# Performance work log

Hardware: AMD Instinct MI355X
Metric: run time of the kernel (lower is better)

## Reference

```python
import jax, jax.numpy as jnp
import numpy as np

N_NODES = 100000
N_EDGES = 1600000
DIM = 128
N_BUNDLES = 8
BUNDLE_DIM = 4
HIDDEN = 256
TIME = 2


def setup_inputs() -> dict:
    key = jax.random.key(0)
    ks = jax.random.split(key, 8)
    x = jax.random.normal(ks[0], (N_NODES, DIM), dtype=jnp.float32)
    node_rep = jax.random.normal(ks[1], (N_NODES, N_BUNDLES, BUNDLE_DIM, BUNDLE_DIM), dtype=jnp.float32)
    # edge list; ensure every node has out-degree >= 1 so degree norm is finite
    src_extra = jax.random.randint(ks[2], (N_EDGES - N_NODES,), 0, N_NODES)
    src = jnp.concatenate([jnp.arange(N_NODES), src_extra]).astype(jnp.int64)
    dst = jax.random.randint(ks[3], (N_EDGES,), 0, N_NODES).astype(jnp.int64)
    w1 = jax.random.normal(ks[4], (HIDDEN, DIM), dtype=jnp.float32) * (1.0 / np.sqrt(DIM))
    b1 = jnp.zeros((HIDDEN,), dtype=jnp.float32)
    w2 = jax.random.normal(ks[5], (DIM, HIDDEN), dtype=jnp.float32) * (1.0 / np.sqrt(HIDDEN))
    b2 = jnp.zeros((DIM,), dtype=jnp.float32)
    return {"x": x, "node_rep": node_rep, "src": src, "dst": dst,
            "w1": w1, "b1": b1, "w2": w2, "b2": b2}


def reference(x, node_rep, src, dst, w1, b1, w2, b2):
    n = x.shape[0]
    # out-degrees (number of edges with node as source)
    deg = jax.ops.segment_sum(jnp.ones_like(src, dtype=x.dtype), src, num_segments=n)
    # u_mul_v: per-edge product of src and dst degrees -> symmetric norm coefs
    norm_coefs = jax.lax.rsqrt(deg[src] * deg[dst])  # [E]
    # per-bundle rotation: einsum('abcd,abde->abce', node_rep, vf)
    vf = x.reshape(n, N_BUNDLES, BUNDLE_DIM, -1)
    vf = jnp.einsum('nbcd,nbde->nbce', node_rep, vf)
    h = vf.reshape(n, DIM)
    # u_mul_e_sum repeated `time` times: out[dst] += h[src] * coef
    for _ in range(TIME):
        h = jax.ops.segment_sum(h[src] * norm_coefs[:, None], dst, num_segments=n)
    # inverse rotation with transposed node_rep
    vf = h.reshape(n, N_BUNDLES, BUNDLE_DIM, -1)
    vf = jnp.einsum('nbdc,nbde->nbce', node_rep, vf)
    h = vf.reshape(n, DIM)
    # feed-forward (dropout=0, exact GELU as in torch nn.GELU default)
    h = jax.nn.gelu(h @ w1.T + b1, approximate=False)
    return h @ w2.T + b2
```

## Files before the change

### kernel.cpp

```cpp
#include <hip/hip_runtime.h>
#include <hip/hip_bf16.h>
#include <math.h>

#define DIM 128
#define HID 256

typedef short s8x __attribute__((ext_vector_type(8)));
typedef float f4x __attribute__((ext_vector_type(4)));

__device__ __forceinline__ unsigned short f2bf(float f) {
    unsigned int u = __float_as_uint(f);
    u += 0x7FFF + ((u >> 16) & 1);
    return (unsigned short)(u >> 16);
}
__device__ __forceinline__ float bf2f(unsigned short b) {
    return __uint_as_float(((unsigned int)b) << 16);
}
__device__ __forceinline__ float bflo(unsigned int p) {
    return __uint_as_float(p << 16);
}
__device__ __forceinline__ float bfhi(unsigned int p) {
    return __uint_as_float(p & 0xffff0000u);
}


__global__ __launch_bounds__(256) void hist_kernel(
        const int* __restrict__ src, const int* __restrict__ dst,
        int* __restrict__ TD, int* __restrict__ TS, int nE, int nbuck, int chunk,
        int NBE) {
    __shared__ int hd[1024], hs[1024];
    const int tid = threadIdx.x, blk = blockIdx.x;
    for (int b = tid; b < nbuck; b += 256) { hd[b] = 0; hs[b] = 0; }
    __syncthreads();
    int beg = blk * chunk, end = min(beg + chunk, nE);
    for (int i = beg + tid; i < end; i += 256) {
        atomicAdd(&hd[dst[i] >> 7], 1);
        atomicAdd(&hs[src[i] >> 7], 1);
    }
    __syncthreads();
    for (int b = tid; b < nbuck; b += 256) {
        TD[b * NBE + blk] = hd[b];
        TS[b * NBE + blk] = hs[b];
    }
}

__global__ void scan_blocks(const int* in, int* out, int* bsums, int n) {
    __shared__ int part[256];
    const int tid = threadIdx.x;
    const int base = blockIdx.x * 1024 + tid * 4;
    int v[4];
    int sum = 0;
#pragma unroll
    for (int k = 0; k < 4; ++k) {
        v[k] = (base + k < n) ? in[base + k] : 0;
        sum += v[k];
    }
    part[tid] = sum;
    __syncthreads();
    for (int off = 1; off < 256; off <<= 1) {
        int t = (tid >= off) ? part[tid - off] : 0;
        __syncthreads();
        part[tid] += t;
        __syncthreads();
    }
    int excl = part[tid] - sum;
    if (tid == 255) bsums[blockIdx.x] = part[255];
#pragma unroll
    for (int k = 0; k < 4; ++k) {
        if (base + k < n) out[base + k] = excl;
        excl += v[k];
    }
}

__global__ void scan_sums(int* bsums, int nb) {
    __shared__ int part[256];
    const int tid = threadIdx.x;
    const int base = tid * 8;
    int v[8];
    int sum = 0;
#pragma unroll
    for (int k = 0; k < 8; ++k) {
        v[k] = (base + k < nb) ? bsums[base + k] : 0;
        sum += v[k];
    }
    part[tid] = sum;
    __syncthreads();
    for (int off = 1; off < 256; off <<= 1) {
        int t = (tid >= off) ? part[tid - off] : 0;
        __syncthreads();
        part[tid] += t;
        __syncthreads();
    }
    int excl = part[tid] - sum;
#pragma unroll
    for (int k = 0; k < 8; ++k) {
        if (base + k < nb) bsums[base + k] = excl;
        excl += v[k];
    }
}

__global__ void scan_add(int* T, const int* __restrict__ bsums, int n2, int half, int E) {
    int i = blockIdx.x * blockDim.x + threadIdx.x;
    if (i < n2) {
        int v = T[i] + bsums[i >> 10];
        T[i] = (i >= half) ? v - E : v;
    }
}

__global__ __launch_bounds__(256) void scatter_edges(
        const int* __restrict__ src, const int* __restrict__ dst,
        const int* __restrict__ TD, const int* __restrict__ TS,
        unsigned int* __restrict__ pairs, unsigned char* __restrict__ sbyte,
        int nE, int nbuck, int chunk, int NBE) {
    __shared__ int cd[1024], cs[1024];
    const int tid = threadIdx.x, blk = blockIdx.x;
    for (int b = tid; b < nbuck; b += 256) {
        cd[b] = TD[b * NBE + blk];
        cs[b] = TS[b * NBE + blk];
    }
    __syncthreads();
    int beg = blk * chunk, end = min(beg + chunk, nE);
    for (int i = beg + tid; i < end; i += 256) {
        int s = src[i], d = dst[i];
        int pd = atomicAdd(&cd[d >> 7], 1);
        pairs[pd] = ((unsigned)s << 7) | (unsigned)(d & 127);
        int ps = atomicAdd(&cs[s >> 7], 1);
        sbyte[ps] = (unsigned char)(s & 127);
    }
}

__global__ __launch_bounds__(256) void finalize_src(
        const unsigned char* __restrict__ sbyte, const int* __restrict__ TS,
        float* __restrict__ rdeg, int nE, int nbuck, int nN, int NBE) {
    __shared__ int hist[128];
    const int tid = threadIdx.x, b = blockIdx.x;
    if (tid < 128) hist[tid] = 0;
    __syncthreads();
    int beg = TS[b * NBE];
    int end = (b + 1 < nbuck) ? TS[(b + 1) * NBE] : nE;
    for (int i = beg + tid; i < end; i += 256)
        atomicAdd(&hist[sbyte[i]], 1);
    __syncthreads();
    if (tid < 128) {
        int idx = (b << 7) + tid;
        if (idx < nN) rdeg[idx] = rsqrtf((float)hist[tid]);
    }
}

template<bool PACK>
__global__ __launch_bounds__(256) void finalize_dst(
        const unsigned int* __restrict__ pairs, const int* __restrict__ TD,
        const float* __restrict__ rdeg,
        int* __restrict__ rowstart, uint2* __restrict__ ecsr,
        int* __restrict__ esrcA, int nE, int nbuck, int nN, int NBE) {
    __shared__ int hist[128], sbuf[128], cur[128];
    const int tid = threadIdx.x, b = blockIdx.x;
    int beg = TD[b * NBE];
    int end = (b + 1 < nbuck) ? TD[(b + 1) * NBE] : nE;
    if (tid < 128) hist[tid] = 0;
    __syncthreads();
    for (int i = beg + tid; i < end; i += 256)
        atomicAdd(&hist[(int)(pairs[i] & 127u)], 1);
    __syncthreads();
    int v = (tid < 128) ? hist[tid] : 0;
    if (tid < 128) sbuf[tid] = v;
    __syncthreads();
    for (int off = 1; off < 128; off <<= 1) {
        int t = (tid < 128 && tid >= off) ? sbuf[tid - off] : 0;
        __syncthreads();
        if (tid < 128) sbuf[tid] += t;
        __syncthreads();
    }
    if (tid < 128) {
        int excl = sbuf[tid] - v;
        cur[tid] = excl;
        int idx = (b << 7) + tid;
        if (idx <= nN) rowstart[idx] = beg + excl;
    }
    __syncthreads();
    for (int i = beg + tid; i < end; i += 256) {
        unsigned int p = pairs[i];
        int l = (int)(p & 127u);
        int s = (int)(p >> 7);
        int pos = atomicAdd(&cur[l], 1);
        if (PACK) {
            float coef = rdeg[s] * rdeg[(b << 7) + l];
            ecsr[beg + pos] = make_uint2((unsigned)s, __float_as_uint(coef));
        } else {
            esrcA[beg + pos] = s;
        }
    }
}

__global__ void rot_cvt_kernel(const float* __restrict__ x, const float* __restrict__ R,
                               unsigned short* __restrict__ h0,
                               const float* __restrict__ w1, const float* __restrict__ w2,
                               unsigned short* __restrict__ w1b, unsigned short* __restrict__ w2b,
                               int n, int nbRot) {
    if ((int)blockIdx.x >= nbRot) {
        int t = (blockIdx.x - nbRot) * 256 + threadIdx.x;
        for (int i = t; i < 32768; i += 4096) {
            w1b[i] = f2bf(w1[i]);
            w2b[i] = f2bf(w2[i]);
        }
        return;
    }
    int u = blockIdx.x * blockDim.x + threadIdx.x;
    if (u >= n * 8) return;
    int nd = u >> 3, b = u & 7;
    const float* xp = &x[(size_t)nd * DIM + b * 16];
    const float* Rp = &R[(size_t)nd * DIM + b * 16];
    float xv[16], rv[16];
#pragma unroll
    for (int d = 0; d < 4; ++d) {
        *(float4*)&xv[d * 4] = *(const float4*)&xp[d * 4];
        *(float4*)&rv[d * 4] = *(const float4*)&Rp[d * 4];
    }
    unsigned short ob[16];
#pragma unroll
    for (int c = 0; c < 4; ++c)
#pragma unroll
        for (int e = 0; e < 4; ++e) {
            float acc = 0.f;
#pragma unroll
            for (int d = 0; d < 4; ++d) acc += rv[c * 4 + d] * xv[d * 4 + e];
            ob[c * 4 + e] = f2bf(acc);
        }
    unsigned short* op = &h0[(size_t)nd * DIM + b * 16];
    *(s8x*)&op[0] = *(s8x*)&ob[0];
    *(s8x*)&op[8] = *(s8x*)&ob[8];
}

template<bool PACK>
__global__ __launch_bounds__(256) void gather_kernel(
        const unsigned short* __restrict__ hsrc,
        const uint2* __restrict__ ecsr, const int* __restrict__ esrcA,
        const float* __restrict__ rdeg, const int* __restrict__ rowstart,
        unsigned short* __restrict__ hdst, int n) {
    const int node = blockIdx.x * 16 + (threadIdx.x >> 4);
    const int lane = threadIdx.x & 15;
    if (node >= n) return;
    const int beg = rowstart[node];
    const int end = rowstart[node + 1];
    float rd = 0.f;
    if (!PACK) rd = rdeg[node];
    float a0 = 0.f, a1 = 0.f, a2 = 0.f, a3 = 0.f;
    float a4 = 0.f, a5 = 0.f, a6 = 0.f, a7 = 0.f;
    int i = beg;
    for (; i + 4 <= end; i += 4) {
        int s0, s1, s2, s3;
        float c0, c1, c2, c3;
        if (PACK) {
            uint2 e0 = ecsr[i], e1 = ecsr[i + 1], e2 = ecsr[i + 2], e3 = ecsr[i + 3];
            s0 = (int)e0.x; c0 = __uint_as_float(e0.y);
            s1 = (int)e1.x; c1 = __uint_as_float(e1.y);
            s2 = (int)e2.x; c2 = __uint_as_float(e2.y);
            s3 = (int)e3.x; c3 = __uint_as_float(e3.y);
        } else {
            s0 = esrcA[i]; s1 = esrcA[i + 1]; s2 = esrcA[i + 2]; s3 = esrcA[i + 3];
            c0 = rdeg[s0] * rd; c1 = rdeg[s1] * rd;
            c2 = rdeg[s2] * rd; c3 = rdeg[s3] * rd;
        }
        uint4 p0 = *(const uint4*)&hsrc[(size_t)s0 * DIM + lane * 8];
        uint4 p1 = *(const uint4*)&hsrc[(size_t)s1 * DIM + lane * 8];
        uint4 p2 = *(const uint4*)&hsrc[(size_t)s2 * DIM + lane * 8];
        uint4 p3 = *(const uint4*)&hsrc[(size_t)s3 * DIM + lane * 8];
        a0 += bflo(p0.x) * c0 + bflo(p1.x) * c1 + bflo(p2.x) * c2 + bflo(p3.x) * c3;
        a1 += bfhi(p0.x) * c0 + bfhi(p1.x) * c1 + bfhi(p2.x) * c2 + bfhi(p3.x) * c3;
        a2 += bflo(p0.y) * c0 + bflo(p1.y) * c1 + bflo(p2.y) * c2 + bflo(p3.y) * c3;
        a3 += bfhi(p0.y) * c0 + bfhi(p1.y) * c1 + bfhi(p2.y) * c2 + bfhi(p3.y) * c3;
        a4 += bflo(p0.z) * c0 + bflo(p1.z) * c1 + bflo(p2.z) * c2 + bflo(p3.z) * c3;
        a5 += bfhi(p0.z) * c0 + bfhi(p1.z) * c1 + bfhi(p2.z) * c2 + bfhi(p3.z) * c3;
        a6 += bflo(p0.w) * c0 + bflo(p1.w) * c1 + bflo(p2.w) * c2 + bflo(p3.w) * c3;
        a7 += bfhi(p0.w) * c0 + bfhi(p1.w) * c1 + bfhi(p2.w) * c2 + bfhi(p3.w) * c3;
    }
    for (; i < end; ++i) {
        int s0;
        float c0;
        if (PACK) {
            uint2 e0 = ecsr[i];
            s0 = (int)e0.x; c0 = __uint_as_float(e0.y);
        } else {
            s0 = esrcA[i];
            c0 = rdeg[s0] * rd;
        }
        uint4 p0 = *(const uint4*)&hsrc[(size_t)s0 * DIM + lane * 8];
        a0 += bflo(p0.x) * c0;
        a1 += bfhi(p0.x) * c0;
        a2 += bflo(p0.y) * c0;
        a3 += bfhi(p0.y) * c0;
        a4 += bflo(p0.z) * c0;
        a5 += bfhi(p0.z) * c0;
        a6 += bflo(p0.w) * c0;
        a7 += bfhi(p0.w) * c0;
    }
    uint4 o;
    o.x = (unsigned)f2bf(a0) | ((unsigned)f2bf(a1) << 16);
    o.y = (unsigned)f2bf(a2) | ((unsigned)f2bf(a3) << 16);
    o.z = (unsigned)f2bf(a4) | ((unsigned)f2bf(a5) << 16);
    o.w = (unsigned)f2bf(a6) | ((unsigned)f2bf(a7) << 16);
    *(uint4*)&hdst[(size_t)node * DIM + lane * 8] = o;
}

#define ABST 136
#define HBST 264
__global__ __launch_bounds__(256, 6) void ffn_kernel(
        const unsigned short* __restrict__ h,
        const float* __restrict__ R,
        const unsigned short* __restrict__ w1b,
        const float* __restrict__ b1,
        const unsigned short* __restrict__ w2b,
        const float* __restrict__ b2,
        float* __restrict__ out, int n) {
    __shared__ unsigned short smem[32 * HBST];
    unsigned short* abuf = smem;
    unsigned short* hbuf = smem;
    const int tid  = threadIdx.x;
    const int node0 = blockIdx.x * 32;
    const int wave = tid >> 6;
    const int lane = tid & 63;
    const int lr = lane & 15;
    const int lq = lane >> 4;

    {
        int nd = tid >> 3, b = tid & 7;
        int gn = node0 + nd;
        float hv[16], rv[16];
        if (gn < n) {
            const unsigned short* hp = &h[(size_t)gn * DIM + b * 16];
            const float* Rp = &R[(size_t)gn * DIM + b * 16];
            unsigned short hraw[16];
            *(s8x*)&hraw[0] = *(const s8x*)&hp[0];
            *(s8x*)&hraw[8] = *(const s8x*)&hp[8];
#pragma unroll
            for (int d = 0; d < 16; ++d) hv[d] = bf2f(hraw[d]);
#pragma unroll
            for (int d = 0; d < 4; ++d)
                *(float4*)&rv[d * 4] = *(const float4*)&Rp[d * 4];
        } else {
#pragma unroll
            for (int d = 0; d < 16; ++d) { hv[d] = 0.f; rv[d] = 0.f; }
        }
#pragma unroll
        for (int c = 0; c < 4; ++c) {
            unsigned short gb[4];
#pragma unroll
            for (int e = 0; e < 4; ++e) {
                float acc = 0.f;
#pragma unroll
                for (int d = 0; d < 4; ++d) acc += rv[d * 4 + c] * hv[d * 4 + e];
                gb[e] = f2bf(acc);
            }
            *(ushort4*)&abuf[nd * ABST + b * 16 + c * 4] =
                make_ushort4(gb[0], gb[1], gb[2], gb[3]);
        }
    }
    __syncthreads();

    f4x acc1[2][4];
#pragma unroll
    for (int mt = 0; mt < 2; ++mt)
#pragma unroll
        for (int nt = 0; nt < 4; ++nt) acc1[mt][nt] = (f4x){0.f, 0.f, 0.f, 0.f};

    const int nw = wave * 64;
    for (int ks = 0; ks < 4; ++ks) {
        const int k0 = ks * 32 + lq * 8;
        s8x af[2], bfv[4];
#pragma unroll
        for (int mt = 0; mt < 2; ++mt)
            af[mt] = *(const s8x*)&abuf[(mt * 16 + lr) * ABST + k0];
#pragma unroll
        for (int nt = 0; nt < 4; ++nt)
            bfv[nt] = *(const s8x*)&w1b[(size_t)(nw + nt * 16 + lr) * 128 + k0];
#pragma unroll
        for (int mt = 0; mt < 2; ++mt)
#pragma unroll
            for (int nt = 0; nt < 4; ++nt)
                acc1[mt][nt] = __builtin_amdgcn_mfma_f32_16x16x32_bf16(
                    af[mt], bfv[nt], acc1[mt][nt], 0, 0, 0);
    }
    __syncthreads();

#pragma unroll
    for (int nt = 0; nt < 4; ++nt) {
        int nn = nw + nt * 16 + lr;
        float bias = b1[nn];
#pragma unroll
        for (int mt = 0; mt < 2; ++mt) {
#pragma unroll
            for (int r = 0; r < 4; ++r) {
                float v = acc1[mt][nt][r] + bias;
                v = 0.5f * v * (1.f + erff(v * 0.70710678118654752f));
                hbuf[(mt * 16 + lq * 4 + r) * HBST + nn] = f2bf(v);
            }
        }
    }
    __syncthreads();

    f4x acc2[2][2];
#pragma unroll
    for (int mt = 0; mt < 2; ++mt)
#pragma unroll
        for (int nt = 0; nt < 2; ++nt) acc2[mt][nt] = (f4x){0.f, 0.f, 0.f, 0.f};

    const int nw2 = wave * 32;
    for (int ks = 0; ks < 8; ++ks) {
        const int k0 = ks * 32 + lq * 8;
        s8x af[2], bf2v[2];
#pragma unroll
        for (int mt = 0; mt < 2; ++mt)
            af[mt] = *(const s8x*)&hbuf[(mt * 16 + lr) * HBST + k0];
#pragma unroll
        for (int nt = 0; nt < 2; ++nt)
            bf2v[nt] = *(const s8x*)&w2b[(size_t)(nw2 + nt * 16 + lr) * 256 + k0];
#pragma unroll
        for (int mt = 0; mt < 2; ++mt)
#pragma unroll
            for (int nt = 0; nt < 2; ++nt)
                acc2[mt][nt] = __builtin_amdgcn_mfma_f32_16x16x32_bf16(
                    af[mt], bf2v[nt], acc2[mt][nt], 0, 0, 0);
    }
#pragma unroll
    for (int nt = 0; nt < 2; ++nt) {
        int n2 = nw2 + nt * 16 + lr;
        float bias = b2[n2];
#pragma unroll
        for (int mt = 0; mt < 2; ++mt) {
#pragma unroll
            for (int r = 0; r < 4; ++r) {
                int gn = node0 + mt * 16 + lq * 4 + r;
                if (gn < n) out[(size_t)gn * DIM + n2] = acc2[mt][nt][r] + bias;
            }
        }
    }
}

extern "C" void kernel_launch(void* const* d_in, const int* in_sizes, int n_in,
                              void* d_out, int out_size, void* d_ws, size_t ws_size,
                              hipStream_t stream) {
    const float* x   = (const float*)d_in[0];
    const float* R   = (const float*)d_in[1];
    const int*   src = (const int*)d_in[2];
    const int*   dst = (const int*)d_in[3];
    const float* w1  = (const float*)d_in[4];
    const float* b1  = (const float*)d_in[5];
    const float* w2  = (const float*)d_in[6];
    const float* b2  = (const float*)d_in[7];
    float* out = (float*)d_out;

    const int N = in_sizes[0] / DIM;
    const int E = in_sizes[2];

    const int nbuck = (N + 127) >> 7;

    const size_t fixed_bytes = (size_t)N * DIM * 4;
    auto tail_bytes = [&](int nbe) {
        return (size_t)N * 4 + (size_t)(N + 1) * 4 +
               (size_t)nbuck * nbe * 8 + 2048 * 4 + (size_t)2 * 32768 * 2;
    };
    int NBE = 1024;
    bool use_pack = true;
    if (fixed_bytes + (size_t)E * 8 + tail_bytes(1024) > ws_size) {
        if (fixed_bytes + (size_t)E * 8 + tail_bytes(256) <= ws_size) {
            NBE = 256;
        } else {
            NBE = 256;
            use_pack = false;
        }
    }
    const int chunk = (E + NBE - 1) / NBE;
    const int nScan = nbuck * NBE;
    const int nScan2 = 2 * nScan;
    const int nbScan2 = (nScan2 + 1023) / 1024;

    unsigned short* hA = (unsigned short*)d_ws;
    unsigned short* hM = hA + (size_t)N * DIM;
    unsigned int*  pairs = (unsigned int*)hM;
    unsigned char* sbyte = (unsigned char*)(pairs + E);
    char* edge_base = (char*)(hM + (size_t)N * DIM);
    const size_t edge_bytes = use_pack ? (size_t)E * 8 : (size_t)E * 4;

    uint2* ecsr  = (uint2*)edge_base;
    int*   esrcA = (int*)edge_base;
    char* q = edge_base + edge_bytes;
    float* rdeg     = (float*)q;
    int*   rowstart = (int*)(rdeg + N);
    int*   TD       = rowstart + (N + 1);
    int*   TS       = TD + nScan;
    int*   bsums    = TS + nScan;
    unsigned short* w1b = (unsigned short*)(bsums + 2048);
    unsigned short* w2b = w1b + 32768;

    const int BLK = 256;

    hist_kernel<<<NBE, BLK, 0, stream>>>(src, dst, TD, TS, E, nbuck, chunk, NBE);
    scan_blocks<<<nbScan2, BLK, 0, stream>>>(TD, TD, bsums, nScan2);
    scan_sums<<<1, BLK, 0, stream>>>(bsums, nbScan2);
    scan_add<<<(nScan2 + BLK - 1) / BLK, BLK, 0, stream>>>(TD, bsums, nScan2, nScan, E);
    scatter_edges<<<NBE, BLK, 0, stream>>>(src, dst, TD, TS, pairs, sbyte, E, nbuck, chunk, NBE);
    finalize_src<<<nbuck, BLK, 0, stream>>>(sbyte, TS, rdeg, E, nbuck, N, NBE);
    if (use_pack)
        finalize_dst<true><<<nbuck, BLK, 0, stream>>>(pairs, TD, rdeg, rowstart,
                                                      ecsr, esrcA, E, nbuck, N, NBE);
    else
        finalize_dst<false><<<nbuck, BLK, 0, stream>>>(pairs, TD, rdeg, rowstart,
                                                       ecsr, esrcA, E, nbuck, N, NBE);

    const int nbRot = ((size_t)N * 8 + BLK - 1) / BLK;
    rot_cvt_kernel<<<nbRot + 16, BLK, 0, stream>>>(x, R, hA, w1, w2, w1b, w2b, N, nbRot);

    const int nbG = (N + 15) / 16;
    if (use_pack) {
        gather_kernel<true><<<nbG, BLK, 0, stream>>>(hA, ecsr, esrcA, rdeg,
                                                     rowstart, hM, N);
        gather_kernel<true><<<nbG, BLK, 0, stream>>>(hM, ecsr, esrcA, rdeg,
                                                     rowstart, hA, N);
    } else {
        gather_kernel<false><<<nbG, BLK, 0, stream>>>(hA, ecsr, esrcA, rdeg,
                                                      rowstart, hM, N);
        gather_kernel<false><<<nbG, BLK, 0, stream>>>(hM, ecsr, esrcA, rdeg,
                                                      rowstart, hA, N);
    }

    ffn_kernel<<<(N + 31) / 32, BLK, 0, stream>>>(hA, R, w1b, b1, w2b, b2, out, N);
}
```

Before: 444.1 us.

## Fuse rotation into histogram kernel, fix NBE=256, enlarge FFN node tile to 64

The rotation/weight-conversion kernel is merged into the histogram launch as extra blocks, which removes one launch and lets the two independent workloads overlap. The histogram block count is fixed at 256 instead of 1024, shrinking the scan arrays. The FFN kernel now processes 64 nodes per block with 4 M-tiles per wave, reusing each weight fragment over more rows, at the cost of doubled LDS and more accumulator registers (occupancy hint lowered to 4).

```diff
diff --git a/kernel.cpp b/kernel.cpp
--- a/kernel.cpp
+++ b/kernel.cpp
@@ -24,12 +24,55 @@
 }
 
 
-__global__ __launch_bounds__(256) void hist_kernel(
+__global__ __launch_bounds__(256) void hist_rot_kernel(
         const int* __restrict__ src, const int* __restrict__ dst,
         int* __restrict__ TD, int* __restrict__ TS, int nE, int nbuck, int chunk,
-        int NBE) {
+        int NBE,
+        const float* __restrict__ x, const float* __restrict__ R,
+        unsigned short* __restrict__ h0,
+        const float* __restrict__ w1, const float* __restrict__ w2,
+        unsigned short* __restrict__ w1b, unsigned short* __restrict__ w2b,
+        int n, int nbRot) {
     __shared__ int hd[1024], hs[1024];
     const int tid = threadIdx.x, blk = blockIdx.x;
+
+    if (blk >= NBE) {
+        const int rb = blk - NBE;
+        if (rb >= nbRot) {
+            int t = (rb - nbRot) * 256 + tid;
+            for (int i = t; i < 32768; i += 4096) {
+                w1b[i] = f2bf(w1[i]);
+                w2b[i] = f2bf(w2[i]);
+            }
+            return;
+        }
+        int u = rb * 256 + tid;
+        if (u >= n * 8) return;
+        int nd = u >> 3, b = u & 7;
+        const float* xp = &x[(size_t)nd * DIM + b * 16];
+        const float* Rp = &R[(size_t)nd * DIM + b * 16];
+        float xv[16], rv[16];
+#pragma unroll
+        for (int d = 0; d < 4; ++d) {
+            *(float4*)&xv[d * 4] = *(const float4*)&xp[d * 4];
+            *(float4*)&rv[d * 4] = *(const float4*)&Rp[d * 4];
+        }
+        unsigned short ob[16];
+#pragma unroll
+        for (int c = 0; c < 4; ++c)
+#pragma unroll
+            for (int e = 0; e < 4; ++e) {
+                float acc = 0.f;
+#pragma unroll
+                for (int d = 0; d < 4; ++d) acc += rv[c * 4 + d] * xv[d * 4 + e];
+                ob[c * 4 + e] = f2bf(acc);
+            }
+        unsigned short* op = &h0[(size_t)nd * DIM + b * 16];
+        *(s8x*)&op[0] = *(s8x*)&ob[0];
+        *(s8x*)&op[8] = *(s8x*)&ob[8];
+        return;
+    }
+
     for (int b = tid; b < nbuck; b += 256) { hd[b] = 0; hs[b] = 0; }
     __syncthreads();
     int beg = blk * chunk, end = min(beg + chunk, nE);
@@ -190,45 +233,6 @@
             esrcA[beg + pos] = s;
         }
     }
-}
-
-__global__ void rot_cvt_kernel(const float* __restrict__ x, const float* __restrict__ R,
-                               unsigned short* __restrict__ h0,
-                               const float* __restrict__ w1, const float* __restrict__ w2,
-                               unsigned short* __restrict__ w1b, unsigned short* __restrict__ w2b,
-                               int n, int nbRot) {
-    if ((int)blockIdx.x >= nbRot) {
-        int t = (blockIdx.x - nbRot) * 256 + threadIdx.x;
-        for (int i = t; i < 32768; i += 4096) {
-            w1b[i] = f2bf(w1[i]);
-            w2b[i] = f2bf(w2[i]);
-        }
-        return;
-    }
-    int u = blockIdx.x * blockDim.x + threadIdx.x;
-    if (u >= n * 8) return;
-    int nd = u >> 3, b = u & 7;
-    const float* xp = &x[(size_t)nd * DIM + b * 16];
-    const float* Rp = &R[(size_t)nd * DIM + b * 16];
-    float xv[16], rv[16];
-#pragma unroll
-    for (int d = 0; d < 4; ++d) {
-        *(float4*)&xv[d * 4] = *(const float4*)&xp[d * 4];
-        *(float4*)&rv[d * 4] = *(const float4*)&Rp[d * 4];
-    }
-    unsigned short ob[16];
-#pragma unroll
-    for (int c = 0; c < 4; ++c)
-#pragma unroll
-        for (int e = 0; e < 4; ++e) {
-            float acc = 0.f;
-#pragma unroll
-            for (int d = 0; d < 4; ++d) acc += rv[c * 4 + d] * xv[d * 4 + e];
-            ob[c * 4 + e] = f2bf(acc);
-        }
-    unsigned short* op = &h0[(size_t)nd * DIM + b * 16];
-    *(s8x*)&op[0] = *(s8x*)&ob[0];
-    *(s8x*)&op[8] = *(s8x*)&ob[8];
 }
 
 template<bool PACK>
@@ -304,7 +308,7 @@
 
 #define ABST 136
 #define HBST 264
-__global__ __launch_bounds__(256, 6) void ffn_kernel(
+__global__ __launch_bounds__(256, 4) void ffn_kernel(
         const unsigned short* __restrict__ h,
         const float* __restrict__ R,
         const unsigned short* __restrict__ w1b,
@@ -312,18 +316,18 @@
         const unsigned short* __restrict__ w2b,
         const float* __restrict__ b2,
         float* __restrict__ out, int n) {
-    __shared__ unsigned short smem[32 * HBST];
+    __shared__ unsigned short smem[64 * HBST];
     unsigned short* abuf = smem;
     unsigned short* hbuf = smem;
     const int tid  = threadIdx.x;
-    const int node0 = blockIdx.x * 32;
+    const int node0 = blockIdx.x * 64;
     const int wave = tid >> 6;
     const int lane = tid & 63;
     const int lr = lane & 15;
     const int lq = lane >> 4;
 
-    {
-        int nd = tid >> 3, b = tid & 7;
+    for (int u = tid; u < 512; u += 256) {
+        int nd = u >> 3, b = u & 7;
         int gn = node0 + nd;
         float hv[16], rv[16];
         if (gn < n) {
@@ -357,24 +361,24 @@
     }
     __syncthreads();
 
-    f4x acc1[2][4];
-#pragma unroll
-    for (int mt = 0; mt < 2; ++mt)
+    f4x acc1[4][4];
+#pragma unroll
+    for (int mt = 0; mt < 4; ++mt)
 #pragma unroll
         for (int nt = 0; nt < 4; ++nt) acc1[mt][nt] = (f4x){0.f, 0.f, 0.f, 0.f};
 
     const int nw = wave * 64;
     for (int ks = 0; ks < 4; ++ks) {
         const int k0 = ks * 32 + lq * 8;
-        s8x af[2], bfv[4];
-#pragma unroll
-        for (int mt = 0; mt < 2; ++mt)
+        s8x af[4], bfv[4];
+#pragma unroll
+        for (int mt = 0; mt < 4; ++mt)
             af[mt] = *(const s8x*)&abuf[(mt * 16 + lr) * ABST + k0];
 #pragma unroll
         for (int nt = 0; nt < 4; ++nt)
             bfv[nt] = *(const s8x*)&w1b[(size_t)(nw + nt * 16 + lr) * 128 + k0];
 #pragma unroll
-        for (int mt = 0; mt < 2; ++mt)
+        for (int mt = 0; mt < 4; ++mt)
 #pragma unroll
             for (int nt = 0; nt < 4; ++nt)
                 acc1[mt][nt] = __builtin_amdgcn_mfma_f32_16x16x32_bf16(
@@ -387,7 +391,7 @@
         int nn = nw + nt * 16 + lr;
         float bias = b1[nn];
 #pragma unroll
-        for (int mt = 0; mt < 2; ++mt) {
+        for (int mt = 0; mt < 4; ++mt) {
 #pragma unroll
             for (int r = 0; r < 4; ++r) {
                 float v = acc1[mt][nt][r] + bias;
@@ -398,24 +402,24 @@
     }
     __syncthreads();
 
-    f4x acc2[2][2];
-#pragma unroll
-    for (int mt = 0; mt < 2; ++mt)
+    f4x acc2[4][2];
+#pragma unroll
+    for (int mt = 0; mt < 4; ++mt)
 #pragma unroll
         for (int nt = 0; nt < 2; ++nt) acc2[mt][nt] = (f4x){0.f, 0.f, 0.f, 0.f};
 
     const int nw2 = wave * 32;
     for (int ks = 0; ks < 8; ++ks) {
         const int k0 = ks * 32 + lq * 8;
-        s8x af[2], bf2v[2];
-#pragma unroll
-        for (int mt = 0; mt < 2; ++mt)
+        s8x af[4], bf2v[2];
+#pragma unroll
+        for (int mt = 0; mt < 4; ++mt)
             af[mt] = *(const s8x*)&hbuf[(mt * 16 + lr) * HBST + k0];
 #pragma unroll
         for (int nt = 0; nt < 2; ++nt)
             bf2v[nt] = *(const s8x*)&w2b[(size_t)(nw2 + nt * 16 + lr) * 256 + k0];
 #pragma unroll
-        for (int mt = 0; mt < 2; ++mt)
+        for (int mt = 0; mt < 4; ++mt)
 #pragma unroll
             for (int nt = 0; nt < 2; ++nt)
                 acc2[mt][nt] = __builtin_amdgcn_mfma_f32_16x16x32_bf16(
@@ -426,7 +430,7 @@
         int n2 = nw2 + nt * 16 + lr;
         float bias = b2[n2];
 #pragma unroll
-        for (int mt = 0; mt < 2; ++mt) {
+        for (int mt = 0; mt < 4; ++mt) {
 #pragma unroll
             for (int r = 0; r < 4; ++r) {
                 int gn = node0 + mt * 16 + lq * 4 + r;
@@ -453,22 +457,7 @@
     const int E = in_sizes[2];
 
     const int nbuck = (N + 127) >> 7;
-
-    const size_t fixed_bytes = (size_t)N * DIM * 4;
-    auto tail_bytes = [&](int nbe) {
-        return (size_t)N * 4 + (size_t)(N + 1) * 4 +
-               (size_t)nbuck * nbe * 8 + 2048 * 4 + (size_t)2 * 32768 * 2;
-    };
-    int NBE = 1024;
-    bool use_pack = true;
-    if (fixed_bytes + (size_t)E * 8 + tail_bytes(1024) > ws_size) {
-        if (fixed_bytes + (size_t)E * 8 + tail_bytes(256) <= ws_size) {
-            NBE = 256;
-        } else {
-            NBE = 256;
-            use_pack = false;
-        }
-    }
+    const int NBE = 256;
     const int chunk = (E + NBE - 1) / NBE;
     const int nScan = nbuck * NBE;
     const int nScan2 = 2 * nScan;
@@ -479,6 +468,11 @@
     unsigned int*  pairs = (unsigned int*)hM;
     unsigned char* sbyte = (unsigned char*)(pairs + E);
     char* edge_base = (char*)(hM + (size_t)N * DIM);
+
+    const size_t tail_bytes = (size_t)N * 4 + (size_t)(N + 1) * 4 +
+                              (size_t)nScan * 8 + 2048 * 4 + (size_t)2 * 32768 * 2;
+    const size_t fixed_bytes = (size_t)N * DIM * 4;
+    const bool use_pack = (fixed_bytes + (size_t)E * 8 + tail_bytes) <= ws_size;
     const size_t edge_bytes = use_pack ? (size_t)E * 8 : (size_t)E * 4;
 
     uint2* ecsr  = (uint2*)edge_base;
@@ -494,7 +488,11 @@
 
     const int BLK = 256;
 
-    hist_kernel<<<NBE, BLK, 0, stream>>>(src, dst, TD, TS, E, nbuck, chunk, NBE);
+    const int nbRot = ((size_t)N * 8 + BLK - 1) / BLK;
+    hist_rot_kernel<<<NBE + nbRot + 16, BLK, 0, stream>>>(
+        src, dst, TD, TS, E, nbuck, chunk, NBE,
+        x, R, hA, w1, w2, w1b, w2b, N, nbRot);
+
     scan_blocks<<<nbScan2, BLK, 0, stream>>>(TD, TD, bsums, nScan2);
     scan_sums<<<1, BLK, 0, stream>>>(bsums, nbScan2);
     scan_add<<<(nScan2 + BLK - 1) / BLK, BLK, 0, stream>>>(TD, bsums, nScan2, nScan, E);
@@ -507,9 +505,6 @@
         finalize_dst<false><<<nbuck, BLK, 0, stream>>>(pairs, TD, rdeg, rowstart,
                                                        ecsr, esrcA, E, nbuck, N, NBE);
 
-    const int nbRot = ((size_t)N * 8 + BLK - 1) / BLK;
-    rot_cvt_kernel<<<nbRot + 16, BLK, 0, stream>>>(x, R, hA, w1, w2, w1b, w2b, N, nbRot);
-
     const int nbG = (N + 15) / 16;
     if (use_pack) {
         gather_kernel<true><<<nbG, BLK, 0, stream>>>(hA, ecsr, esrcA, rdeg,
@@ -523,5 +518,5 @@
                                                       rowstart, hA, N);
     }
 
-    ffn_kernel<<<(N + 31) / 32, BLK, 0, stream>>>(hA, R, w1b, b1, w2b, b2, out, N);
-}
+    ffn_kernel<<<(N + 63) / 64, BLK, 0, stream>>>(hA, R, w1b, b1, w2b, b2, out, N);
+}
```

Measured after the change: 416.9 us. 6.1% less time.
